# Kernel optimization log

Measured on AMD Instinct MI355X. Metric: run time of the kernel, lower is better.

Reference implementation:

```python
import jax, jax.numpy as jnp
import numpy as np

KS = 3                      # kernel side
GRID_SIZE = 5
SPLINE_ORDER = 3
N_CONVS = 8
IN_FEAT = KS * KS           # KANLinear in_features per patch
NCOEF = GRID_SIZE + SPLINE_ORDER  # number of B-spline basis functions


def setup_inputs() -> dict:
    key = jax.random.key(0)
    k1, k2, k3, k4 = jax.random.split(key, 4)
    x = jax.random.normal(k1, (8, 32, 64, 64), jnp.float32)
    # efficient-kan KANLinear params, stacked over the n_convs independent kernels
    base_weight = jax.random.normal(k2, (N_CONVS, IN_FEAT), jnp.float32) / np.sqrt(IN_FEAT).astype(np.float32)
    spline_weight = jax.random.normal(k3, (N_CONVS, IN_FEAT, NCOEF), jnp.float32) * 0.1
    spline_scaler = jax.random.normal(k4, (N_CONVS, IN_FEAT), jnp.float32) / np.sqrt(IN_FEAT).astype(np.float32)
    # knot grid: uniform over grid_range=[-1,1], extended by spline_order on each side
    h = 2.0 / GRID_SIZE
    g = jnp.arange(-SPLINE_ORDER, GRID_SIZE + SPLINE_ORDER + 1, dtype=jnp.float32) * h - 1.0
    grid = jnp.tile(g[None, :], (IN_FEAT, 1))  # [in, G+2k+1]
    return {"x": x, "base_weight": base_weight, "spline_weight": spline_weight,
            "spline_scaler": spline_scaler, "grid": grid}


def b_splines(x, grid):
    # x: [..., in], grid: [in, G+2k+1] -> bases [..., in, G+k]  (Cox-de Boor)
    xe = x[..., None]
    bases = ((xe >= grid[:, :-1]) & (xe < grid[:, 1:])).astype(x.dtype)
    for k in range(1, SPLINE_ORDER + 1):
        left = (xe - grid[:, :-(k + 1)]) / (grid[:, k:-1] - grid[:, :-(k + 1)])
        right = (grid[:, k + 1:] - xe) / (grid[:, k + 1:] - grid[:, 1:-k])
        bases = left * bases[..., :-1] + right * bases[..., 1:]
    return bases


def reference(x, base_weight, spline_weight, spline_scaler, grid):
    B, C, H, W = x.shape
    ho, wo = H - KS + 1, W - KS + 1  # stride 1, dilation 1, no padding
    # im2col: [B, C*KS*KS, ho, wo], channel-major feature order (matches torch Unfold)
    patches = jax.lax.conv_general_dilated_patches(x, (KS, KS), (1, 1), 'VALID')
    patches = patches.reshape(B, C, IN_FEAT, ho * wo).transpose(0, 1, 3, 2)  # [B,C,L,in]
    # KANLinear(out_features=1) applied per conv n over each patch
    base = jnp.einsum('bcli,ni->bcnl', jax.nn.silu(patches), base_weight)
    basis = b_splines(patches, grid)                     # [B,C,L,in,coef]
    sw = spline_weight * spline_scaler[..., None]        # scaled spline weight [n,in,coef]
    spl = jnp.einsum('bclis,nis->bcnl', basis, sw)
    # output channel index = kern + channel * n_convs (channel-major)
    return (base + spl).reshape(B, C * N_CONVS, ho, wo)
```

## Files before the change

### kernel.cpp

```cpp
#include <hip/hip_runtime.h>
#include <hip/hip_bf16.h>


#define N_CONVS 8
#define HH 64
#define WW 64
#define HO 62
#define WO 62
#define BAND 16
#define LROWS 18
#define LW 65

__global__ __launch_bounds__(256, 3) void kan_fused(
    const float* __restrict__ x,
    const float* __restrict__ bw,
    const float* __restrict__ sw,
    const float* __restrict__ sc,
    const float* __restrict__ grid,
    float* __restrict__ out)
{
    __shared__ float feat[LROWS * LW * 9];

    const int blk  = blockIdx.x;
    const int band = blk & 3;
    const int img  = blk >> 2;
    const int r0   = band * BAND;
    const int nr   = (HO - r0) < BAND ? (HO - r0) : BAND;
    const int nin  = (HH - r0) < LROWS ? (HH - r0) : LROWS;

    float g[12];
#pragma unroll
    for (int j = 0; j < 12; j++) g[j] = grid[j];
    float i1[11], i2[10], i3[9];
#pragma unroll
    for (int j = 0; j < 11; j++) i1[j] = __builtin_amdgcn_rcpf(g[j + 1] - g[j]);
#pragma unroll
    for (int j = 0; j < 10; j++) i2[j] = __builtin_amdgcn_rcpf(g[j + 2] - g[j]);
#pragma unroll
    for (int j = 0; j < 9; j++)  i3[j] = __builtin_amdgcn_rcpf(g[j + 3] - g[j]);

    const float* xb = x + (size_t)img * (HH * WW) + (size_t)r0 * WW;
    for (int p = threadIdx.x; p < nin * WW; p += 256) {
        const int r = p >> 6, c = p & 63;
        const float xv = xb[p];

        const float s0 = xv * __builtin_amdgcn_rcpf(1.0f + __expf(-xv));

        float ee[12], d[12];
#pragma unroll
        for (int j = 0; j < 12; j++) {
            ee[j] = xv - g[j];
            d[j]  = (xv >= g[j]) ? 1.0f : 0.0f;
        }
        float b0[11];
#pragma unroll
        for (int j = 0; j < 11; j++) b0[j] = d[j] - d[j + 1];
        float b1[10];
#pragma unroll
        for (int j = 0; j < 10; j++)
            b1[j] = (ee[j] * i1[j]) * b0[j] - (ee[j + 2] * i1[j + 1]) * b0[j + 1];
        float b2[9];
#pragma unroll
        for (int j = 0; j < 9; j++)
            b2[j] = (ee[j] * i2[j]) * b1[j] - (ee[j + 3] * i2[j + 1]) * b1[j + 1];
        float b3[8];
#pragma unroll
        for (int j = 0; j < 8; j++)
            b3[j] = (ee[j] * i3[j]) * b2[j] - (ee[j + 4] * i3[j + 1]) * b2[j + 1];

        float* f = &feat[(r * LW + c) * 9];
        f[0] = s0;
#pragma unroll
        for (int j = 0; j < 8; j++) f[j + 1] = b3[j];
    }
    __syncthreads();

    const int row = threadIdx.x >> 4;
    const int xs  = (threadIdx.x & 15) * 4;
    if (row < nr) {
        float acc[N_CONVS][4];
#pragma unroll
        for (int n = 0; n < N_CONVS; n++)
#pragma unroll
            for (int t = 0; t < 4; t++) acc[n][t] = 0.0f;

#pragma unroll 1
        for (int ky = 0; ky < 3; ky++) {
            float fw[6][9];
#pragma unroll
            for (int c6 = 0; c6 < 6; c6++) {
                const float* fp = &feat[((row + ky) * LW + xs + c6) * 9];
#pragma unroll
                for (int j = 0; j < 9; j++) fw[c6][j] = fp[j];
            }
#pragma unroll
            for (int kx = 0; kx < 3; kx++) {
                const int i = ky * 3 + kx;
#pragma unroll
                for (int n = 0; n < N_CONVS; n++) {
                    const float scv = sc[n * 9 + i];
                    const float bwv = bw[n * 9 + i];
                    const float* swp = sw + ((n * 9 + i) << 3);
                    float s[4];
#pragma unroll
                    for (int t = 0; t < 4; t++) s[t] = swp[0] * fw[kx + t][1];
#pragma unroll
                    for (int j = 1; j < 8; j++) {
                        const float w = swp[j];
#pragma unroll
                        for (int t = 0; t < 4; t++)
                            s[t] = fmaf(w, fw[kx + t][j + 1], s[t]);
                    }
#pragma unroll
                    for (int t = 0; t < 4; t++) {
                        acc[n][t] = fmaf(scv, s[t], acc[n][t]);
                        acc[n][t] = fmaf(bwv, fw[kx + t][0], acc[n][t]);
                    }
                }
            }
        }

        const int oy = r0 + row;
        float* ob = out + (size_t)img * N_CONVS * (HO * WO) + oy * WO + xs;
#pragma unroll
        for (int n = 0; n < N_CONVS; n++) {
            float* o = ob + n * (HO * WO);
            *(float2*)o = make_float2(acc[n][0], acc[n][1]);
            if (xs < 58) *(float2*)(o + 2) = make_float2(acc[n][2], acc[n][3]);
        }
    }
}

extern "C" void kernel_launch(void* const* d_in, const int* in_sizes, int n_in,
                              void* d_out, int out_size, void* d_ws, size_t ws_size,
                              hipStream_t stream) {
    const float* x    = (const float*)d_in[0];
    const float* bw   = (const float*)d_in[1];
    const float* sw   = (const float*)d_in[2];
    const float* sc   = (const float*)d_in[3];
    const float* grid = (const float*)d_in[4];
    float* out = (float*)d_out;

    kan_fused<<<256 * 4, 256, 0, stream>>>(x, bw, sw, sc, grid, out);
}
```

Before: 95.47 us.

## Use closed-form uniform cubic B-spline, planar LDS layout, and prefolded weights

Replaces the full Cox-de Boor recursion with a closed-form uniform cubic B-spline that computes only the 4 nonzero bases from the knot interval index. This assumes the grid is uniform, using only grid[0] and grid[1]. Shared memory moves from interleaved per-pixel features to separate feature planes, so the inner loop can use vectorized float4/float2 LDS reads. A small prep kernel folds spline_scaler into spline_weight and packs the base weights into one table, at the cost of an extra launch and reliance on the workspace.

```diff
diff --git a/kernel.cpp b/kernel.cpp
--- a/kernel.cpp
+++ b/kernel.cpp
@@ -9,17 +9,34 @@
 #define WO 62
 #define BAND 16
 #define LROWS 18
-#define LW 65
+#define PW 68
+#define PLANE (LROWS * PW)
 
-__global__ __launch_bounds__(256, 3) void kan_fused(
+__global__ __launch_bounds__(768) void kan_prep(const float* __restrict__ bw,
+                                                const float* __restrict__ sw,
+                                                const float* __restrict__ sc,
+                                                float* __restrict__ wf) {
+    const int t   = threadIdx.x;
+    const int blk = t >> 5;
+    const int r   = t & 31;
+    const int ky  = blk >> 3, n = blk & 7;
+    const int kx  = r / 10, j = r % 10;
+    float v = 0.0f;
+    if (kx < 3 && j <= 8) {
+        const int i = ky * 3 + kx;
+        v = (j == 0) ? bw[n * 9 + i]
+                     : sw[(n * 9 + i) * 8 + (j - 1)] * sc[n * 9 + i];
+    }
+    wf[t] = v;
+}
+
+__global__ __launch_bounds__(256, 3) void kan_main(
     const float* __restrict__ x,
-    const float* __restrict__ bw,
-    const float* __restrict__ sw,
-    const float* __restrict__ sc,
     const float* __restrict__ grid,
+    const float* __restrict__ wf,
     float* __restrict__ out)
 {
-    __shared__ float feat[LROWS * LW * 9];
+    __shared__ __align__(16) float feat[9 * PLANE];
 
     const int blk  = blockIdx.x;
     const int band = blk & 3;
@@ -28,55 +45,41 @@
     const int nr   = (HO - r0) < BAND ? (HO - r0) : BAND;
     const int nin  = (HH - r0) < LROWS ? (HH - r0) : LROWS;
 
-    float g[12];
-#pragma unroll
-    for (int j = 0; j < 12; j++) g[j] = grid[j];
-    float i1[11], i2[10], i3[9];
-#pragma unroll
-    for (int j = 0; j < 11; j++) i1[j] = __builtin_amdgcn_rcpf(g[j + 1] - g[j]);
-#pragma unroll
-    for (int j = 0; j < 10; j++) i2[j] = __builtin_amdgcn_rcpf(g[j + 2] - g[j]);
-#pragma unroll
-    for (int j = 0; j < 9; j++)  i3[j] = __builtin_amdgcn_rcpf(g[j + 3] - g[j]);
+    const float g0   = grid[0];
+    const float invh = __builtin_amdgcn_rcpf(grid[1] - grid[0]);
 
     const float* xb = x + (size_t)img * (HH * WW) + (size_t)r0 * WW;
     for (int p = threadIdx.x; p < nin * WW; p += 256) {
         const int r = p >> 6, c = p & 63;
         const float xv = xb[p];
 
-        const float s0 = xv * __builtin_amdgcn_rcpf(1.0f + __expf(-xv));
+        float* fp = &feat[r * PW + c];
+        fp[0] = xv * __builtin_amdgcn_rcpf(1.0f + __expf(-xv));
+#pragma unroll
+        for (int j = 1; j < 9; j++) fp[j * PLANE] = 0.0f;
 
-        float ee[12], d[12];
+        const float u0 = (xv - g0) * invh;
+        const int   m  = (int)floorf(u0);
+        if (m >= 0 && m <= 10) {
+            const float u  = u0 - (float)m;
+            const float um = 1.0f - u;
+            const float u2 = u * u, u3 = u2 * u;
+            const float N0 = um * um * um * (1.0f / 6.0f);
+            const float N1 = (3.0f * u3 - 6.0f * u2 + 4.0f) * (1.0f / 6.0f);
+            const float N2 = (-3.0f * u3 + 3.0f * u2 + 3.0f * u + 1.0f) * (1.0f / 6.0f);
+            const float N3 = u3 * (1.0f / 6.0f);
+            const float Nv[4] = {N0, N1, N2, N3};
 #pragma unroll
-        for (int j = 0; j < 12; j++) {
-            ee[j] = xv - g[j];
-            d[j]  = (xv >= g[j]) ? 1.0f : 0.0f;
+            for (int s = 0; s < 4; s++) {
+                const int j = m - 3 + s;
+                if (j >= 0 && j <= 7) fp[(j + 1) * PLANE] = Nv[s];
+            }
         }
-        float b0[11];
-#pragma unroll
-        for (int j = 0; j < 11; j++) b0[j] = d[j] - d[j + 1];
-        float b1[10];
-#pragma unroll
-        for (int j = 0; j < 10; j++)
-            b1[j] = (ee[j] * i1[j]) * b0[j] - (ee[j + 2] * i1[j + 1]) * b0[j + 1];
-        float b2[9];
-#pragma unroll
-        for (int j = 0; j < 9; j++)
-            b2[j] = (ee[j] * i2[j]) * b1[j] - (ee[j + 3] * i2[j + 1]) * b1[j + 1];
-        float b3[8];
-#pragma unroll
-        for (int j = 0; j < 8; j++)
-            b3[j] = (ee[j] * i3[j]) * b2[j] - (ee[j + 4] * i3[j + 1]) * b2[j + 1];
-
-        float* f = &feat[(r * LW + c) * 9];
-        f[0] = s0;
-#pragma unroll
-        for (int j = 0; j < 8; j++) f[j + 1] = b3[j];
     }
     __syncthreads();
 
     const int row = threadIdx.x >> 4;
-    const int xs  = (threadIdx.x & 15) * 4;
+    const int xs  = (threadIdx.x & 15) << 2;
     if (row < nr) {
         float acc[N_CONVS][4];
 #pragma unroll
@@ -86,35 +89,29 @@
 
 #pragma unroll 1
         for (int ky = 0; ky < 3; ky++) {
-            float fw[6][9];
+            float fw[9][6];
 #pragma unroll
-            for (int c6 = 0; c6 < 6; c6++) {
-                const float* fp = &feat[((row + ky) * LW + xs + c6) * 9];
+            for (int j = 0; j < 9; j++) {
+                const float* pl = &feat[j * PLANE + (row + ky) * PW + xs];
+                const float4 a = *(const float4*)pl;
+                const float2 b = *(const float2*)(pl + 4);
+                fw[j][0] = a.x; fw[j][1] = a.y; fw[j][2] = a.z;
+                fw[j][3] = a.w; fw[j][4] = b.x; fw[j][5] = b.y;
+            }
+            const float* wk = wf + (ky << 8);
 #pragma unroll
-                for (int j = 0; j < 9; j++) fw[c6][j] = fp[j];
-            }
+            for (int n = 0; n < N_CONVS; n++) {
+                const float* wn = wk + (n << 5);
 #pragma unroll
-            for (int kx = 0; kx < 3; kx++) {
-                const int i = ky * 3 + kx;
-#pragma unroll
-                for (int n = 0; n < N_CONVS; n++) {
-                    const float scv = sc[n * 9 + i];
-                    const float bwv = bw[n * 9 + i];
-                    const float* swp = sw + ((n * 9 + i) << 3);
-                    float s[4];
-#pragma unroll
-                    for (int t = 0; t < 4; t++) s[t] = swp[0] * fw[kx + t][1];
-#pragma unroll
-                    for (int j = 1; j < 8; j++) {
-                        const float w = swp[j];
-#pragma unroll
-                        for (int t = 0; t < 4; t++)
-                            s[t] = fmaf(w, fw[kx + t][j + 1], s[t]);
-                    }
+                for (int kx = 0; kx < 3; kx++) {
+                    const float* gg = wn + kx * 10;
 #pragma unroll
                     for (int t = 0; t < 4; t++) {
-                        acc[n][t] = fmaf(scv, s[t], acc[n][t]);
-                        acc[n][t] = fmaf(bwv, fw[kx + t][0], acc[n][t]);
+                        float a = acc[n][t];
+#pragma unroll
+                        for (int j = 0; j < 9; j++)
+                            a = fmaf(gg[j], fw[j][kx + t], a);
+                        acc[n][t] = a;
                     }
                 }
             }
@@ -140,6 +137,8 @@
     const float* sc   = (const float*)d_in[3];
     const float* grid = (const float*)d_in[4];
     float* out = (float*)d_out;
+    float* wf  = (float*)d_ws;
 
-    kan_fused<<<256 * 4, 256, 0, stream>>>(x, bw, sw, sc, grid, out);
+    kan_prep<<<1, 768, 0, stream>>>(bw, sw, sc, wf);
+    kan_main<<<256 * 4, 256, 0, stream>>>(x, grid, wf, out);
 }
```

Measured after the change: 96.45 us. About the same (+1.0%).
